# Performance work log

Hardware: AMD Instinct MI355X
Metric: run time of the kernel (lower is better)

Reference implementation:

```python
import jax, jax.numpy as jnp
import numpy as np

HIDDEN = 256
B, L = 4, 4096


def setup_inputs() -> dict:
    key = jax.random.key(0)
    k_in, k_q, k_k, k_v, k_len = jax.random.split(key, 5)
    inputs = jax.random.normal(k_in, (B, L, HIDDEN), dtype=jnp.float32)
    # torch.rand -> uniform [0,1)
    W_query = jax.random.uniform(k_q, (HIDDEN, HIDDEN), dtype=jnp.float32)
    W_key = jax.random.uniform(k_k, (HIDDEN, HIDDEN), dtype=jnp.float32)
    W_value = jax.random.uniform(k_v, (HIDDEN, HIDDEN), dtype=jnp.float32)
    lengths = jax.random.randint(k_len, (B,), 1, L + 1, dtype=jnp.int64)
    return {"inputs": inputs, "W_query": W_query, "W_key": W_key,
            "W_value": W_value, "lengths": lengths}


def reference(inputs, W_query, W_key, W_value, lengths):
    # lengths is unused by the original module (no masking applied).
    # QKV projections (batched matmul with shared weight)
    queries = jnp.einsum('blh,hd->bld', inputs, W_query)
    keys = jnp.einsum('blh,hd->bld', inputs, W_key)
    values = jnp.einsum('blh,hd->bld', inputs, W_value)
    # scaled dot-product attention, full [B, L, L] scores as in original
    scale = 1.0 / jnp.sqrt(jnp.asarray(HIDDEN, dtype=inputs.dtype))
    attn_scores = jnp.einsum('bqd,bkd->bqk', queries, keys) * scale
    attentions = jax.nn.softmax(attn_scores, axis=-1)
    weighted = jnp.einsum('bqk,bkd->bqd', attentions, values)
    return weighted
```

## Files before the change

### kernel.cpp

```cpp
#include <hip/hip_runtime.h>


typedef __bf16 bf16x8 __attribute__((ext_vector_type(8)));
typedef _Float16 f16x8 __attribute__((ext_vector_type(8)));
typedef _Float16 f16x4 __attribute__((ext_vector_type(4)));
typedef float floatx4 __attribute__((ext_vector_type(4)));

#define MFMA16B(a, b, c) __builtin_amdgcn_mfma_f32_16x16x32_bf16(a, b, c, 0, 0, 0)
#define MFMA16F(a, b, c) __builtin_amdgcn_mfma_f32_16x16x32_f16(a, b, c, 0, 0, 0)
#define GLOAD_LDS16(g, l)                                                  \
  __builtin_amdgcn_global_load_lds(                                        \
      (const __attribute__((address_space(1))) void *)(g),                 \
      (__attribute__((address_space(3))) void *)(l), 16, 0, 0)

#define HID 256
#define LSEQ 4096
#define NB 4
#define NTOK (NB * LSEQ)
#define PLANE ((size_t)NTOK * HID)
#define NSPLIT 4
#define QSCALE 0.09016844005556021f


__device__ __forceinline__ void split_bf16(float v, __bf16 &h, __bf16 &l) {
  h = (__bf16)v;
  l = (__bf16)(v - (float)h);
}

template <int N>
__device__ __forceinline__ float dpp_ror(float v) {
  return __builtin_bit_cast(float,
      __builtin_amdgcn_update_dpp(0, __builtin_bit_cast(int, v),
                                  0x120 + N, 0xf, 0xf, true));
}
__device__ __forceinline__ float row_sum16(float v) {
  v += dpp_ror<1>(v);
  v += dpp_ror<2>(v);
  v += dpp_ror<4>(v);
  v += dpp_ror<8>(v);
  return v;
}
__device__ __forceinline__ float row_max16(float v) {
  v = fmaxf(v, dpp_ror<1>(v));
  v = fmaxf(v, dpp_ror<2>(v));
  v = fmaxf(v, dpp_ror<4>(v));
  v = fmaxf(v, dpp_ror<8>(v));
  return v;
}

__global__ __launch_bounds__(256) void wsplit(const float *__restrict__ Wq,
                                              const float *__restrict__ Wk,
                                              const float *__restrict__ Wv,
                                              __bf16 *__restrict__ Wht,
                                              __bf16 *__restrict__ Wlt) {
  __shared__ float tile[32][256];
  const int wsel = blockIdx.x;
  const int hb = blockIdx.y;
  const float *W = (wsel == 0) ? Wq : (wsel == 1) ? Wk : Wv;
  __bf16 *oh = Wht + wsel * HID * HID;
  __bf16 *ol = Wlt + wsel * HID * HID;
  const int t = threadIdx.x;
  #pragma unroll
  for (int p = 0; p < 8; ++p) {
    int r = p * 4 + (t >> 6);
    int c = (t & 63) * 4;
    *(floatx4 *)&tile[r][c] = *(const floatx4 *)&W[(hb * 32 + r) * HID + c];
  }
  __syncthreads();
  #pragma unroll
  for (int q = 0; q < 4; ++q) {
    int n = q * 64 + (t >> 2);
    int hs = (t & 3) * 8;
    bf16x8 hh, ll;
    #pragma unroll
    for (int i = 0; i < 8; ++i) {
      float v = tile[hs + i][n];
      __bf16 h, l;
      split_bf16(v, h, l);
      hh[i] = h; ll[i] = l;
    }
    *(bf16x8 *)&oh[n * HID + hb * 32 + hs] = hh;
    *(bf16x8 *)&ol[n * HID + hb * 32 + hs] = ll;
  }
}

__global__ __launch_bounds__(256, 2) void qkv_proj(const float *__restrict__ X,
                                                   const __bf16 *__restrict__ Wht,
                                                   const __bf16 *__restrict__ Wlt,
                                                   _Float16 *__restrict__ Qf,
                                                   _Float16 *__restrict__ Kf,
                                                   _Float16 *__restrict__ Vf) {
  __shared__ __bf16 WhS[64 * 256];
  __shared__ __bf16 WlS[64 * 256];
  _Float16 *Tf = (_Float16 *)WhS;

  const int mtile = blockIdx.x;
  const int col0 = blockIdx.y * 64;
  const int tid = threadIdx.x;
  const int w4 = tid >> 6;
  const int lane = tid & 63;
  const int quad = lane >> 4;
  const int ln = lane & 15;
  const int arow = mtile * 64 + w4 * 16 + ln;

  bf16x8 ah[8], al[8];
  #pragma unroll
  for (int kc = 0; kc < 8; ++kc) {
    const float *xp = X + (size_t)arow * HID + kc * 32 + quad * 8;
    floatx4 x0 = *(const floatx4 *)xp;
    floatx4 x1 = *(const floatx4 *)(xp + 4);
    #pragma unroll
    for (int j = 0; j < 4; ++j) {
      __bf16 h, l;
      split_bf16(x0[j], h, l); ah[kc][j] = h; al[kc][j] = l;
      split_bf16(x1[j], h, l); ah[kc][4 + j] = h; al[kc][4 + j] = l;
    }
  }

  const int srow = tid >> 2;
  const int sseg = tid & 3;

  bf16x8 pwh[8], pwl[8];
  {
    const size_t wbase = (size_t)(col0 + srow) * HID;
    #pragma unroll
    for (int j = 0; j < 8; ++j) {
      const int chunk = j * 4 + sseg;
      pwh[j] = *(const bf16x8 *)&Wht[wbase + chunk * 8];
      pwl[j] = *(const bf16x8 *)&Wlt[wbase + chunk * 8];
    }
  }

  for (int w = 0; w < 3; ++w) {
    __syncthreads();
    #pragma unroll
    for (int j = 0; j < 8; ++j) {
      const int chunk = j * 4 + sseg;
      const int dst = srow * 256 + ((chunk ^ (srow & 7)) << 3);
      *(bf16x8 *)&WhS[dst] = pwh[j];
      *(bf16x8 *)&WlS[dst] = pwl[j];
    }
    __syncthreads();

    if (w < 2) {
      const size_t wbase = (size_t)(w + 1) * HID * HID + (size_t)(col0 + srow) * HID;
      #pragma unroll
      for (int j = 0; j < 8; ++j) {
        const int chunk = j * 4 + sseg;
        pwh[j] = *(const bf16x8 *)&Wht[wbase + chunk * 8];
        pwl[j] = *(const bf16x8 *)&Wlt[wbase + chunk * 8];
      }
    }

    floatx4 acc[4] = {};
    #pragma unroll
    for (int kc = 0; kc < 8; ++kc) {
      #pragma unroll
      for (int nt = 0; nt < 4; ++nt) {
        const int a = (nt * 16 + ln) * 256 + (((kc * 4 + quad) ^ (ln & 7)) << 3);
        bf16x8 bh = *(const bf16x8 *)&WhS[a];
        bf16x8 bl = *(const bf16x8 *)&WlS[a];
        acc[nt] = MFMA16B(ah[kc], bh, acc[nt]);
        acc[nt] = MFMA16B(ah[kc], bl, acc[nt]);
        acc[nt] = MFMA16B(al[kc], bh, acc[nt]);
      }
    }

    if (w == 0) {
      #pragma unroll
      for (int nt = 0; nt < 4; ++nt) {
        #pragma unroll
        for (int r = 0; r < 4; ++r) {
          const int orow = mtile * 64 + w4 * 16 + quad * 4 + r;
          const int ocol = col0 + nt * 16 + ln;
          Qf[(size_t)orow * HID + ocol] = (_Float16)(acc[nt][r] * QSCALE);
        }
      }
    } else if (w == 1) {
      __syncthreads();
      #pragma unroll
      for (int nt = 0; nt < 4; ++nt) {
        #pragma unroll
        for (int r = 0; r < 4; ++r) {
          const int tok_l = w4 * 16 + quad * 4 + r;
          const int h_l = nt * 16 + ln;
          Tf[tok_l * 72 + h_l] = (_Float16)acc[nt][r];
        }
      }
      __syncthreads();
      #pragma unroll
      for (int i = 0; i < 2; ++i) {
        const int c = i * 256 + tid;
        const int lane_f = c & 63;
        const int ntf = (c >> 6) & 1;
        const int kcL = (c >> 7) & 1;
        const int t2 = (c >> 8) & 1;
        const int qf = lane_f >> 4;
        const int lnf = lane_f & 15;
        const int tok_l = t2 * 32 + ntf * 16 + lnf;
        f16x8 v = *(const f16x8 *)&Tf[tok_l * 72 + kcL * 32 + qf * 8];
        const int T = mtile * 2 + t2;
        const int kc = (col0 >> 5) + kcL;
        *(f16x8 *)&Kf[(size_t)T * 8192 + ((ntf * 8 + kc) * 64 + lane_f) * 8] = v;
      }
    } else {
      __syncthreads();
      #pragma unroll
      for (int nt = 0; nt < 4; ++nt) {
        #pragma unroll
        for (int r = 0; r < 4; ++r) {
          const int tok_l = w4 * 16 + quad * 4 + r;
          const int d_l = nt * 16 + ln;
          Tf[d_l * 72 + tok_l] = (_Float16)acc[nt][r];
        }
      }
      __syncthreads();
      #pragma unroll
      for (int i = 0; i < 2; ++i) {
        const int c = i * 256 + tid;
        const int lane_f = c & 63;
        const int dtL = (c >> 6) & 3;
        const int t2 = (c >> 8) & 1;
        const int qf = lane_f >> 4;
        const int lnf = lane_f & 15;
        const int d_l = dtL * 16 + lnf;
        f16x8 v = *(const f16x8 *)&Tf[d_l * 72 + t2 * 32 + qf * 8];
        const int T = mtile * 2 + t2;
        const int dt = (col0 >> 4) + dtL;
        *(f16x8 *)&Vf[(size_t)(T * 16 + dt) * 512 + lane_f * 8] = v;
      }
    }
  }
}

__global__ __launch_bounds__(256, 2) void attn(const _Float16 *__restrict__ Qf,
                                               const _Float16 *__restrict__ Kf,
                                               const _Float16 *__restrict__ Vf,
                                               _Float16 *__restrict__ Op,
                                               float *__restrict__ Mp,
                                               float *__restrict__ Lp) {
  __shared__ _Float16 KS0[8192];
  __shared__ _Float16 KS1[8192];
  __shared__ _Float16 PsS[4 * 16 * 40];

  const int bx = blockIdx.x;
  const int ks = bx & 3;
  const int qt = bx >> 2;
  const int b = qt >> 6;
  const int qtl = qt & 63;
  const int tid = threadIdx.x;
  const int w4 = tid >> 6;
  const int lane = tid & 63;
  const int quad = lane >> 4;
  const int ln = lane & 15;
  const int T0 = b * 128 + ks * 32;

  const int qtok = b * LSEQ + qtl * 64 + w4 * 16 + ln;
  f16x8 q[8];
  #pragma unroll
  for (int kc = 0; kc < 8; ++kc)
    q[kc] = *(const f16x8 *)&Qf[(size_t)qtok * HID + kc * 32 + quad * 8];

  const _Float16 *kuni = Kf + (size_t)T0 * 8192;
  const _Float16 *vuni = Vf + (size_t)T0 * 8192;
  const int koff = tid * 8;
  const int voff = lane * 8;

  #pragma unroll
  for (int i = 0; i < 4; ++i)
    GLOAD_LDS16(kuni + i * 2048 + koff, &KS0[i * 2048 + koff]);

  float m[4] = {-1e30f, -1e30f, -1e30f, -1e30f};
  float l[4] = {0.f, 0.f, 0.f, 0.f};
  floatx4 o[16] = {};

  for (int jm = 0; jm < 16; ++jm) {
    floatx4 s[4];
    __syncthreads();
    {
      const _Float16 *src = kuni + (size_t)(2 * jm + 1) * 8192 + koff;
      #pragma unroll
      for (int i = 0; i < 4; ++i)
        GLOAD_LDS16(src + i * 2048, &KS1[i * 2048 + koff]);
    }
    {
      floatx4 pa[2] = {}, pb[2] = {};
      __builtin_amdgcn_s_setprio(1);
      #pragma unroll
      for (int nt = 0; nt < 2; ++nt)
        #pragma unroll
        for (int kc = 0; kc < 4; ++kc) {
          pa[nt] = MFMA16F(q[kc], *(const f16x8 *)(KS0 + (nt * 8 + kc) * 512 + voff), pa[nt]);
          pb[nt] = MFMA16F(q[4 + kc], *(const f16x8 *)(KS0 + (nt * 8 + 4 + kc) * 512 + voff), pb[nt]);
        }
      __builtin_amdgcn_s_setprio(0);
      s[0] = pa[0] + pb[0];
      s[1] = pa[1] + pb[1];
    }
    __syncthreads();
    if (jm < 15) {
      const _Float16 *src = kuni + (size_t)(2 * jm + 2) * 8192 + koff;
      #pragma unroll
      for (int i = 0; i < 4; ++i)
        GLOAD_LDS16(src + i * 2048, &KS0[i * 2048 + koff]);
    }
    const _Float16 *va = vuni + (size_t)(2 * jm) * 8192;
    const _Float16 *vbp = vuni + (size_t)(2 * jm + 1) * 8192;
    f16x8 vb0[8];
    #pragma unroll
    for (int dt = 0; dt < 8; ++dt)
      vb0[dt] = *(const f16x8 *)(va + dt * 512 + voff);
    {
      floatx4 pa[2] = {}, pb[2] = {};
      __builtin_amdgcn_s_setprio(1);
      #pragma unroll
      for (int nt = 0; nt < 2; ++nt)
        #pragma unroll
        for (int kc = 0; kc < 4; ++kc) {
          pa[nt] = MFMA16F(q[kc], *(const f16x8 *)(KS1 + (nt * 8 + kc) * 512 + voff), pa[nt]);
          pb[nt] = MFMA16F(q[4 + kc], *(const f16x8 *)(KS1 + (nt * 8 + 4 + kc) * 512 + voff), pb[nt]);
        }
      __builtin_amdgcn_s_setprio(0);
      s[2] = pa[0] + pb[0];
      s[3] = pa[1] + pb[1];
    }
    f16x8 vb1[8];
    #pragma unroll
    for (int dt = 0; dt < 8; ++dt)
      vb1[dt] = *(const f16x8 *)(va + (8 + dt) * 512 + voff);

    float alpha[4];
    #pragma unroll
    for (int r = 0; r < 4; ++r) {
      const float tmax = row_max16(
          fmaxf(fmaxf(s[0][r], s[1][r]), fmaxf(s[2][r], s[3][r])));
      const float mn = fmaxf(m[r], tmax);
      const float al = exp2f(m[r] - mn);
      const float p0 = exp2f(s[0][r] - mn);
      const float p1 = exp2f(s[1][r] - mn);
      const float p2 = exp2f(s[2][r] - mn);
      const float p3 = exp2f(s[3][r] - mn);
      s[0][r] = p0; s[1][r] = p1; s[2][r] = p2; s[3][r] = p3;
      const float rs = row_sum16((p0 + p1) + (p2 + p3));
      l[r] = l[r] * al + rs;
      m[r] = mn;
      alpha[r] = al;
    }

    _Float16 *ps = PsS + w4 * (16 * 40);
    #pragma unroll
    for (int nt = 0; nt < 2; ++nt)
      #pragma unroll
      for (int r = 0; r < 4; ++r)
        ps[(quad * 4 + r) * 40 + nt * 16 + ln] = (_Float16)s[nt][r];

    const float amin = fminf(fminf(alpha[0], alpha[1]), fminf(alpha[2], alpha[3]));
    if (__any(amin < 1.0f)) {
      #pragma unroll
      for (int dt = 0; dt < 16; ++dt) {
        o[dt][0] *= alpha[0]; o[dt][1] *= alpha[1];
        o[dt][2] *= alpha[2]; o[dt][3] *= alpha[3];
      }
    }

    const f16x8 paA = *(const f16x8 *)&ps[ln * 40 + quad * 8];

    __builtin_amdgcn_s_setprio(1);
    #pragma unroll
    for (int dt = 0; dt < 8; ++dt) o[dt] = MFMA16F(paA, vb0[dt], o[dt]);
    __builtin_amdgcn_s_setprio(0);
    f16x8 vb2[8];
    #pragma unroll
    for (int dt = 0; dt < 8; ++dt)
      vb2[dt] = *(const f16x8 *)(vbp + dt * 512 + voff);
    __builtin_amdgcn_s_setprio(1);
    #pragma unroll
    for (int dt = 0; dt < 8; ++dt) o[8 + dt] = MFMA16F(paA, vb1[dt], o[8 + dt]);
    __builtin_amdgcn_s_setprio(0);
    f16x8 vb3[8];
    #pragma unroll
    for (int dt = 0; dt < 8; ++dt)
      vb3[dt] = *(const f16x8 *)(vbp + (8 + dt) * 512 + voff);

    #pragma unroll
    for (int nt = 0; nt < 2; ++nt)
      #pragma unroll
      for (int r = 0; r < 4; ++r)
        ps[(quad * 4 + r) * 40 + nt * 16 + ln] = (_Float16)s[2 + nt][r];

    const f16x8 paB = *(const f16x8 *)&ps[ln * 40 + quad * 8];

    __builtin_amdgcn_s_setprio(1);
    #pragma unroll
    for (int dt = 0; dt < 8; ++dt) o[dt] = MFMA16F(paB, vb2[dt], o[dt]);
    #pragma unroll
    for (int dt = 0; dt < 8; ++dt) o[8 + dt] = MFMA16F(paB, vb3[dt], o[8 + dt]);
    __builtin_amdgcn_s_setprio(0);
  }

  const int rowbase = b * LSEQ + qtl * 64 + w4 * 16 + quad * 4;
  #pragma unroll
  for (int dt = 0; dt < 16; ++dt)
    #pragma unroll
    for (int r = 0; r < 4; ++r)
      Op[(size_t)ks * PLANE + (size_t)(rowbase + r) * HID + dt * 16 + ln] =
          (_Float16)o[dt][r];
  if (ln == 0) {
    #pragma unroll
    for (int r = 0; r < 4; ++r) {
      Mp[ks * NTOK + rowbase + r] = m[r];
      Lp[ks * NTOK + rowbase + r] = l[r];
    }
  }
}

__global__ __launch_bounds__(256) void merge(const _Float16 *__restrict__ Op,
                                             const float *__restrict__ Mp,
                                             const float *__restrict__ Lp,
                                             float *__restrict__ Out) {
  const int row = blockIdx.x * 4 + (threadIdx.x >> 6);
  const int c = (threadIdx.x & 63) * 4;
  float ms[NSPLIT], ls[NSPLIT];
  #pragma unroll
  for (int s = 0; s < NSPLIT; ++s) {
    ms[s] = Mp[s * NTOK + row];
    ls[s] = Lp[s * NTOK + row];
  }
  const float M = fmaxf(fmaxf(ms[0], ms[1]), fmaxf(ms[2], ms[3]));
  float e[NSPLIT], den = 0.f;
  #pragma unroll
  for (int s = 0; s < NSPLIT; ++s) {
    e[s] = exp2f(ms[s] - M);
    den += ls[s] * e[s];
  }
  const float inv = 1.0f / den;
  floatx4 out = {};
  #pragma unroll
  for (int s = 0; s < NSPLIT; ++s) {
    const f16x4 a = *(const f16x4 *)&Op[(size_t)s * PLANE + (size_t)row * HID + c];
    const float w = e[s] * inv;
    #pragma unroll
    for (int i = 0; i < 4; ++i) out[i] += w * (float)a[i];
  }
  *(floatx4 *)&Out[(size_t)row * HID + c] = out;
}

extern "C" void kernel_launch(void *const *d_in, const int *in_sizes, int n_in,
                              void *d_out, int out_size, void *d_ws, size_t ws_size,
                              hipStream_t stream) {
  const float *X = (const float *)d_in[0];
  const float *Wq = (const float *)d_in[1];
  const float *Wk = (const float *)d_in[2];
  const float *Wv = (const float *)d_in[3];

  _Float16 *ws = (_Float16 *)d_ws;
  _Float16 *Qf = ws;
  _Float16 *Kf = Qf + PLANE;
  _Float16 *Vf = Kf + PLANE;
  __bf16 *Wht = (__bf16 *)(Vf + PLANE);
  __bf16 *Wlt = Wht + 3 * HID * HID;
  _Float16 *Op = (_Float16 *)(Wlt + 3 * HID * HID);
  float *Mp = (float *)(Op + NSPLIT * PLANE);
  float *Lp = Mp + NSPLIT * NTOK;

  wsplit<<<dim3(3, 8), 256, 0, stream>>>(Wq, Wk, Wv, Wht, Wlt);
  qkv_proj<<<dim3(256, 4), 256, 0, stream>>>(X, Wht, Wlt, Qf, Kf, Vf);
  attn<<<NTOK / 64 * NSPLIT, 256, 0, stream>>>(Qf, Kf, Vf, Op, Mp, Lp);
  merge<<<NTOK / 4, 256, 0, stream>>>(Op, Mp, Lp, (float *)d_out);
}
```

Before: 220.3 us.

## Stage V tiles through LDS with double-buffered K/V async pipeline

New measurement: 226.7 us. 2.9% more time.

```diff
diff --git a/kernel.cpp b/kernel.cpp
--- a/kernel.cpp
+++ b/kernel.cpp
@@ -239,8 +239,8 @@
                                                _Float16 *__restrict__ Op,
                                                float *__restrict__ Mp,
                                                float *__restrict__ Lp) {
-  __shared__ _Float16 KS0[8192];
-  __shared__ _Float16 KS1[8192];
+  __shared__ _Float16 KS[2][8192];
+  __shared__ _Float16 VS[2][8192];
   __shared__ _Float16 PsS[4 * 16 * 40];
 
   const int bx = blockIdx.x;
@@ -268,135 +268,100 @@
 
   #pragma unroll
   for (int i = 0; i < 4; ++i)
-    GLOAD_LDS16(kuni + i * 2048 + koff, &KS0[i * 2048 + koff]);
+    GLOAD_LDS16(kuni + i * 2048 + koff, &KS[0][i * 2048 + koff]);
+  #pragma unroll
+  for (int i = 0; i < 4; ++i)
+    GLOAD_LDS16(vuni + i * 2048 + koff, &VS[0][i * 2048 + koff]);
+  #pragma unroll
+  for (int i = 0; i < 4; ++i)
+    GLOAD_LDS16(kuni + 8192 + i * 2048 + koff, &KS[1][i * 2048 + koff]);
+  #pragma unroll
+  for (int i = 0; i < 4; ++i)
+    GLOAD_LDS16(vuni + 8192 + i * 2048 + koff, &VS[1][i * 2048 + koff]);
 
   float m[4] = {-1e30f, -1e30f, -1e30f, -1e30f};
   float l[4] = {0.f, 0.f, 0.f, 0.f};
   floatx4 o[16] = {};
-
-  for (int jm = 0; jm < 16; ++jm) {
-    floatx4 s[4];
-    __syncthreads();
-    {
-      const _Float16 *src = kuni + (size_t)(2 * jm + 1) * 8192 + koff;
-      #pragma unroll
-      for (int i = 0; i < 4; ++i)
-        GLOAD_LDS16(src + i * 2048, &KS1[i * 2048 + koff]);
-    }
-    {
-      floatx4 pa[2] = {}, pb[2] = {};
-      __builtin_amdgcn_s_setprio(1);
-      #pragma unroll
-      for (int nt = 0; nt < 2; ++nt)
-        #pragma unroll
-        for (int kc = 0; kc < 4; ++kc) {
-          pa[nt] = MFMA16F(q[kc], *(const f16x8 *)(KS0 + (nt * 8 + kc) * 512 + voff), pa[nt]);
-          pb[nt] = MFMA16F(q[4 + kc], *(const f16x8 *)(KS0 + (nt * 8 + 4 + kc) * 512 + voff), pb[nt]);
-        }
-      __builtin_amdgcn_s_setprio(0);
-      s[0] = pa[0] + pb[0];
-      s[1] = pa[1] + pb[1];
-    }
-    __syncthreads();
-    if (jm < 15) {
-      const _Float16 *src = kuni + (size_t)(2 * jm + 2) * 8192 + koff;
-      #pragma unroll
-      for (int i = 0; i < 4; ++i)
-        GLOAD_LDS16(src + i * 2048, &KS0[i * 2048 + koff]);
-    }
-    const _Float16 *va = vuni + (size_t)(2 * jm) * 8192;
-    const _Float16 *vbp = vuni + (size_t)(2 * jm + 1) * 8192;
-    f16x8 vb0[8];
-    #pragma unroll
-    for (int dt = 0; dt < 8; ++dt)
-      vb0[dt] = *(const f16x8 *)(va + dt * 512 + voff);
-    {
-      floatx4 pa[2] = {}, pb[2] = {};
-      __builtin_amdgcn_s_setprio(1);
-      #pragma unroll
-      for (int nt = 0; nt < 2; ++nt)
-        #pragma unroll
-        for (int kc = 0; kc < 4; ++kc) {
-          pa[nt] = MFMA16F(q[kc], *(const f16x8 *)(KS1 + (nt * 8 + kc) * 512 + voff), pa[nt]);
-          pb[nt] = MFMA16F(q[4 + kc], *(const f16x8 *)(KS1 + (nt * 8 + 4 + kc) * 512 + voff), pb[nt]);
-        }
-      __builtin_amdgcn_s_setprio(0);
-      s[2] = pa[0] + pb[0];
-      s[3] = pa[1] + pb[1];
-    }
-    f16x8 vb1[8];
-    #pragma unroll
-    for (int dt = 0; dt < 8; ++dt)
-      vb1[dt] = *(const f16x8 *)(va + (8 + dt) * 512 + voff);
-
-    float alpha[4];
-    #pragma unroll
-    for (int r = 0; r < 4; ++r) {
-      const float tmax = row_max16(
-          fmaxf(fmaxf(s[0][r], s[1][r]), fmaxf(s[2][r], s[3][r])));
-      const float mn = fmaxf(m[r], tmax);
-      const float al = exp2f(m[r] - mn);
-      const float p0 = exp2f(s[0][r] - mn);
-      const float p1 = exp2f(s[1][r] - mn);
-      const float p2 = exp2f(s[2][r] - mn);
-      const float p3 = exp2f(s[3][r] - mn);
-      s[0][r] = p0; s[1][r] = p1; s[2][r] = p2; s[3][r] = p3;
-      const float rs = row_sum16((p0 + p1) + (p2 + p3));
-      l[r] = l[r] * al + rs;
-      m[r] = mn;
-      alpha[r] = al;
-    }
-
-    _Float16 *ps = PsS + w4 * (16 * 40);
-    #pragma unroll
-    for (int nt = 0; nt < 2; ++nt)
-      #pragma unroll
-      for (int r = 0; r < 4; ++r)
-        ps[(quad * 4 + r) * 40 + nt * 16 + ln] = (_Float16)s[nt][r];
-
-    const float amin = fminf(fminf(alpha[0], alpha[1]), fminf(alpha[2], alpha[3]));
-    if (__any(amin < 1.0f)) {
-      #pragma unroll
-      for (int dt = 0; dt < 16; ++dt) {
-        o[dt][0] *= alpha[0]; o[dt][1] *= alpha[1];
-        o[dt][2] *= alpha[2]; o[dt][3] *= alpha[3];
-      }
-    }
-
-    const f16x8 paA = *(const f16x8 *)&ps[ln * 40 + quad * 8];
-
-    __builtin_amdgcn_s_setprio(1);
-    #pragma unroll
-    for (int dt = 0; dt < 8; ++dt) o[dt] = MFMA16F(paA, vb0[dt], o[dt]);
-    __builtin_amdgcn_s_setprio(0);
-    f16x8 vb2[8];
-    #pragma unroll
-    for (int dt = 0; dt < 8; ++dt)
-      vb2[dt] = *(const f16x8 *)(vbp + dt * 512 + voff);
-    __builtin_amdgcn_s_setprio(1);
-    #pragma unroll
-    for (int dt = 0; dt < 8; ++dt) o[8 + dt] = MFMA16F(paA, vb1[dt], o[8 + dt]);
-    __builtin_amdgcn_s_setprio(0);
-    f16x8 vb3[8];
-    #pragma unroll
-    for (int dt = 0; dt < 8; ++dt)
-      vb3[dt] = *(const f16x8 *)(vbp + (8 + dt) * 512 + voff);
-
-    #pragma unroll
-    for (int nt = 0; nt < 2; ++nt)
-      #pragma unroll
-      for (int r = 0; r < 4; ++r)
-        ps[(quad * 4 + r) * 40 + nt * 16 + ln] = (_Float16)s[2 + nt][r];
-
-    const f16x8 paB = *(const f16x8 *)&ps[ln * 40 + quad * 8];
-
-    __builtin_amdgcn_s_setprio(1);
-    #pragma unroll
-    for (int dt = 0; dt < 8; ++dt) o[dt] = MFMA16F(paB, vb2[dt], o[dt]);
-    #pragma unroll
-    for (int dt = 0; dt < 8; ++dt) o[8 + dt] = MFMA16F(paB, vb3[dt], o[8 + dt]);
-    __builtin_amdgcn_s_setprio(0);
-  }
+  _Float16 *ps = PsS + w4 * (16 * 40);
+
+#define ATTN_TILE(TT, BUF, WAITN, DOISSUE)                                   \
+  {                                                                          \
+    asm volatile("s_waitcnt vmcnt(" #WAITN ")" ::: "memory");                \
+    __builtin_amdgcn_s_barrier();                                            \
+    __builtin_amdgcn_sched_barrier(0);                                       \
+    const _Float16 *Kb = KS[BUF];                                            \
+    const _Float16 *Vb = VS[BUF];                                            \
+    floatx4 s0, s1;                                                          \
+    {                                                                        \
+      floatx4 pa0 = {}, pb0 = {}, pa1 = {}, pb1 = {};                        \
+      __builtin_amdgcn_s_setprio(1);                                         \
+      _Pragma("unroll")                                                      \
+      for (int kc = 0; kc < 4; ++kc) {                                       \
+        pa0 = MFMA16F(q[kc], *(const f16x8 *)(Kb + kc * 512 + voff), pa0);   \
+        pb0 = MFMA16F(q[4 + kc], *(const f16x8 *)(Kb + (4 + kc) * 512 + voff), pb0); \
+        pa1 = MFMA16F(q[kc], *(const f16x8 *)(Kb + (8 + kc) * 512 + voff), pa1);     \
+        pb1 = MFMA16F(q[4 + kc], *(const f16x8 *)(Kb + (12 + kc) * 512 + voff), pb1);\
+      }                                                                      \
+      __builtin_amdgcn_s_setprio(0);                                         \
+      s0 = pa0 + pb0;                                                        \
+      s1 = pa1 + pb1;                                                        \
+    }                                                                        \
+    float alpha[4];                                                          \
+    _Pragma("unroll")                                                        \
+    for (int r = 0; r < 4; ++r) {                                            \
+      const float tmax = row_max16(fmaxf(s0[r], s1[r]));                     \
+      const float mn = fmaxf(m[r], tmax);                                    \
+      const float al = exp2f(m[r] - mn);                                     \
+      const float p0 = exp2f(s0[r] - mn);                                    \
+      const float p1 = exp2f(s1[r] - mn);                                    \
+      s0[r] = p0; s1[r] = p1;                                                \
+      l[r] = l[r] * al + row_sum16(p0 + p1);                                 \
+      m[r] = mn;                                                             \
+      alpha[r] = al;                                                         \
+    }                                                                        \
+    _Pragma("unroll")                                                        \
+    for (int r = 0; r < 4; ++r) {                                            \
+      ps[(quad * 4 + r) * 40 + ln] = (_Float16)s0[r];                        \
+      ps[(quad * 4 + r) * 40 + 16 + ln] = (_Float16)s1[r];                   \
+    }                                                                        \
+    const float amin =                                                       \
+        fminf(fminf(alpha[0], alpha[1]), fminf(alpha[2], alpha[3]));         \
+    if (__any(amin < 1.0f)) {                                                \
+      _Pragma("unroll")                                                      \
+      for (int dt = 0; dt < 16; ++dt) {                                      \
+        o[dt][0] *= alpha[0]; o[dt][1] *= alpha[1];                          \
+        o[dt][2] *= alpha[2]; o[dt][3] *= alpha[3];                          \
+      }                                                                      \
+    }                                                                        \
+    const f16x8 paf = *(const f16x8 *)&ps[ln * 40 + quad * 8];               \
+    __builtin_amdgcn_s_setprio(1);                                           \
+    _Pragma("unroll")                                                        \
+    for (int dt = 0; dt < 16; ++dt)                                          \
+      o[dt] = MFMA16F(paf, *(const f16x8 *)(Vb + dt * 512 + voff), o[dt]);   \
+    __builtin_amdgcn_s_setprio(0);                                           \
+    __builtin_amdgcn_sched_barrier(0);                                       \
+    __builtin_amdgcn_s_barrier();                                            \
+    __builtin_amdgcn_sched_barrier(0);                                       \
+    if (DOISSUE) {                                                           \
+      const _Float16 *ksrc = kuni + (size_t)(TT + 2) * 8192 + koff;          \
+      const _Float16 *vsrc = vuni + (size_t)(TT + 2) * 8192 + koff;          \
+      _Pragma("unroll")                                                      \
+      for (int i = 0; i < 4; ++i)                                            \
+        GLOAD_LDS16(ksrc + i * 2048, &KS[BUF][i * 2048 + koff]);             \
+      _Pragma("unroll")                                                      \
+      for (int i = 0; i < 4; ++i)                                            \
+        GLOAD_LDS16(vsrc + i * 2048, &VS[BUF][i * 2048 + koff]);             \
+    }                                                                        \
+  }
+
+  for (int jm = 0; jm < 15; ++jm) {
+    const int t0 = 2 * jm;
+    ATTN_TILE(t0, 0, 8, 1)
+    ATTN_TILE(t0 + 1, 1, 8, 1)
+  }
+  ATTN_TILE(30, 0, 8, 0)
+  ATTN_TILE(31, 1, 0, 0)
+#undef ATTN_TILE
 
   const int rowbase = b * LSEQ + qtl * 64 + w4 * 16 + quad * 4;
   #pragma unroll
```
